# Optimization experiments

Measured on AMD Instinct MI355X. Metric: run time of the kernel, lower is better.

The kernel has to match this reference:

```python
import jax, jax.numpy as jnp
import numpy as np

ELEM, EMBD = 512, 512

def setup_inputs() -> dict:
    key = jax.random.key(0)
    ks = jax.random.split(key, 7)
    s = 1.0 / np.sqrt(ELEM)
    return {
        "x": jax.random.normal(ks[0], (8, 2048, ELEM), dtype=jnp.float32),
        "Wq": jax.random.normal(ks[1], (ELEM, EMBD), dtype=jnp.float32) * s,
        "bq": jnp.zeros((EMBD,), dtype=jnp.float32),
        "Wk": jax.random.normal(ks[2], (ELEM, EMBD), dtype=jnp.float32) * s,
        "bk": jnp.zeros((EMBD,), dtype=jnp.float32),
        "Wv": jax.random.normal(ks[3], (ELEM, EMBD), dtype=jnp.float32) * s,
        "bv": jnp.zeros((EMBD,), dtype=jnp.float32),
    }

def reference(x, Wq, bq, Wk, bk, Wv, bv):
    # x: [N, S, E]
    q = x @ Wq + bq            # [N, S, D]
    k = x @ Wk + bk            # [N, S, D]
    v = x @ Wv + bv            # [N, S, D]
    # NOTE: original has no 1/sqrt(d) scaling.
    logits = jnp.einsum('nsd,ntd->nst', q, k)   # [N, S, S]
    attn = jax.nn.softmax(logits, axis=-1)
    return jnp.einsum('nst,ntd->nsd', attn, v)  # [N, S, D]
```

## Files before the change

### kernel.cpp

```cpp
#include <hip/hip_runtime.h>
#include <hip/hip_fp16.h>

#define SEQ 2048
#define DIM 512

typedef __attribute__((ext_vector_type(8))) short short8;
typedef __attribute__((ext_vector_type(4))) float f32x4;
typedef _Float16 h8 __attribute__((ext_vector_type(8)));
typedef _Float16 h4 __attribute__((ext_vector_type(4)));

#define MFMA16(a, b, c) __builtin_amdgcn_mfma_f32_16x16x32_f16((a), (b), (c), 0, 0, 0)

#define GLOAD_LDS16(g, l)                                                              \
    __builtin_amdgcn_global_load_lds(                                                  \
        (const __attribute__((address_space(1))) unsigned int*)(g),                    \
        (__attribute__((address_space(3))) unsigned int*)(l), 16, 0, 0)

template <int MODE>
__global__ __launch_bounds__(256) void gemmc(
    const _Float16* __restrict__ A, const _Float16* __restrict__ B,
    const float* __restrict__ bq, const float* __restrict__ bk,
    const float* __restrict__ bv,
    _Float16* __restrict__ oq, _Float16* __restrict__ ok, _Float16* __restrict__ ovt,
    float* __restrict__ of, int bat0) {
    __shared__ char sm[2 * 32768];
    constexpr int T  = (MODE == 0) ? 16 : (MODE == 1) ? 8 : 32;
    constexpr int PA = (MODE == 0) ? 512 : (MODE == 1) ? 512 : 4096;
    constexpr int PB = (MODE == 0) ? 1024 : (MODE == 1) ? 512 : 2048;

    int tid = threadIdx.x, wid = tid >> 6, lane = tid & 63, r = lane & 15, g = lane >> 4;
    int mw = wid >> 1, nw = wid & 1;
    int m0 = blockIdx.x * 128, n0 = blockIdx.y * 128, bz = blockIdx.z;

    const _Float16 *Ab, *Bb;
    if (MODE == 0) {
        Ab = A + (size_t)m0 * 512;
        Bb = B + (size_t)n0 * 1024;
    } else if (MODE == 1) {
        int b = bat0 + bz;
        Ab = A + ((size_t)(b * SEQ) + m0) * 512;
        Bb = B + ((size_t)(b * SEQ) + n0) * 512;
    } else {
        int b = bat0 + bz;
        Ab = A + (size_t)bz * (SEQ * 4096) + (size_t)m0 * 4096;
        Bb = B + (size_t)b * (512 * SEQ) + (size_t)n0 * 2048;
    }

    const char* gA[4];
    const char* gB[4];
    int ldsw[4];
#pragma unroll
    for (int j = 0; j < 4; ++j) {
        int ci = (j * 4 + wid) * 64 + lane;
        int row = ci >> 3, cl = ci & 7;
        int col16 = cl ^ (row & 7);
        gA[j] = (const char*)Ab + (size_t)row * (PA * 2) + col16 * 16;
        gB[j] = (const char*)Bb + (size_t)row * (PB * 2) + col16 * 16;
        ldsw[j] = (j * 4 + wid) * 1024;
    }
    int offA[4][2], offB[4][2];
#pragma unroll
    for (int m = 0; m < 4; ++m) {
        int rowA = mw * 64 + m * 16 + r;
        int rowB = nw * 64 + m * 16 + r;
#pragma unroll
        for (int ks = 0; ks < 2; ++ks) {
            offA[m][ks] = rowA * 128 + (((ks * 4 + g) ^ (rowA & 7)) * 16);
            offB[m][ks] = rowB * 128 + (((ks * 4 + g) ^ (rowB & 7)) * 16);
        }
    }

    f32x4 acc[4][4];
#pragma unroll
    for (int m = 0; m < 4; ++m)
#pragma unroll
        for (int n = 0; n < 4; ++n) acc[m][n] = (f32x4)(0.0f);

    auto STG = [&](int t, int b) {
        int ka = (MODE == 0) ? ((t & 7) * 128) : (t * 128);
        int kb = t * 128;
        char* dA = sm + b * 32768;
        char* dB = sm + b * 32768 + 16384;
#pragma unroll
        for (int j = 0; j < 4; ++j) {
            GLOAD_LDS16(gA[j] + ka, dA + ldsw[j]);
            GLOAD_LDS16(gB[j] + kb, dB + ldsw[j]);
        }
    };

    STG(0, 0);
    asm volatile("s_waitcnt vmcnt(0)" ::: "memory");
    __builtin_amdgcn_s_barrier();

#pragma unroll
    for (int t = 0; t < T; ++t) {
        const int buf = t & 1;
        if (t + 1 < T) STG(t + 1, buf ^ 1);
        const char* bA = sm + buf * 32768;
        const char* bB = sm + buf * 32768 + 16384;
        h8 af[4][2], bf[4][2];
#pragma unroll
        for (int m = 0; m < 4; ++m)
#pragma unroll
            for (int ks = 0; ks < 2; ++ks) {
                af[m][ks] = *(const h8*)(bA + offA[m][ks]);
                bf[m][ks] = *(const h8*)(bB + offB[m][ks]);
            }
#pragma unroll
        for (int ks = 0; ks < 2; ++ks)
#pragma unroll
            for (int m = 0; m < 4; ++m)
#pragma unroll
                for (int n = 0; n < 4; ++n)
                    acc[m][n] = MFMA16(af[m][ks], bf[n][ks], acc[m][n]);
        if (t + 1 < T) {
            asm volatile("s_waitcnt vmcnt(0)" ::: "memory");
            __builtin_amdgcn_s_barrier();
        }
    }

    if (MODE == 0) {
        int p = n0 >> 9;
        int ncl = n0 & 511;
        const float* bias = (p == 0) ? bq : (p == 1) ? bk : bv;
#pragma unroll
        for (int n = 0; n < 4; ++n) {
            int col = ncl + nw * 64 + n * 16 + r;
            float bi = bias[col];
#pragma unroll
            for (int m = 0; m < 4; ++m) {
                int grow0 = m0 + mw * 64 + m * 16 + 4 * g;
                if (p == 0) {
                    for (int reg = 0; reg < 4; ++reg)
                        oq[(size_t)(grow0 + reg) * 512 + col] =
                            (_Float16)(acc[m][n][reg] + bi);
                } else if (p == 1) {
                    for (int reg = 0; reg < 4; ++reg)
                        ok[(size_t)(grow0 + reg) * 512 + col] =
                            (_Float16)(acc[m][n][reg] + bi);
                } else {
                    int b = grow0 >> 11, s0 = grow0 & 2047;
                    h4 pv;
                    pv[0] = (_Float16)(acc[m][n][0] + bi);
                    pv[1] = (_Float16)(acc[m][n][1] + bi);
                    pv[2] = (_Float16)(acc[m][n][2] + bi);
                    pv[3] = (_Float16)(acc[m][n][3] + bi);
                    *(h4*)(&ovt[(size_t)b * (512 * 2048) + (size_t)col * 2048 + s0]) = pv;
                }
            }
        }
    } else if (MODE == 1) {
        float* sb = of + (size_t)bz * (SEQ * (size_t)SEQ);
#pragma unroll
        for (int n = 0; n < 4; ++n) {
            int col = n0 + nw * 64 + n * 16 + r;
#pragma unroll
            for (int m = 0; m < 4; ++m) {
                int grow0 = m0 + mw * 64 + m * 16 + 4 * g;
                for (int reg = 0; reg < 4; ++reg)
                    sb[(size_t)(grow0 + reg) * SEQ + col] = acc[m][n][reg];
            }
        }
    } else {
        int b = bat0 + bz;
#pragma unroll
        for (int n = 0; n < 4; ++n) {
            int col = n0 + nw * 64 + n * 16 + r;
#pragma unroll
            for (int m = 0; m < 4; ++m) {
                int grow0 = m0 + mw * 64 + m * 16 + 4 * g;
                for (int reg = 0; reg < 4; ++reg)
                    of[(size_t)(b * SEQ + grow0 + reg) * 512 + col] = acc[m][n][reg];
            }
        }
    }
}

__global__ __launch_bounds__(256) void k0a_splitw(
    const float* __restrict__ Wq, const float* __restrict__ Wk, const float* __restrict__ Wv,
    _Float16* __restrict__ wstk) {
    int idx = blockIdx.x * 256 + threadIdx.x;
    int p = idx >> 18;
    int rem = idx & 262143;
    int k = rem >> 9, n = rem & 511;
    const float* W = (p == 0) ? Wq : (p == 1) ? Wk : Wv;
    float w = W[rem];
    _Float16 h = (_Float16)w;
    size_t base = (size_t)(p * 512 + n) * 1024;
    wstk[base + k] = h;
    wstk[base + 512 + k] = (_Float16)(w - (float)h);
}

__global__ __launch_bounds__(256) void k0b_splitx(
    const float* __restrict__ x, _Float16* __restrict__ xh) {
    size_t i = (size_t)(blockIdx.x * 256 + threadIdx.x) * 4;
    float4 v = *(const float4*)(x + i);
    h4 h;
    h[0] = (_Float16)v.x; h[1] = (_Float16)v.y;
    h[2] = (_Float16)v.z; h[3] = (_Float16)v.w;
    *(h4*)(xh + i) = h;
}

__global__ __launch_bounds__(256) void k3_softmax(float* __restrict__ sbuf) {
    size_t row = blockIdx.x;
    float* srow = sbuf + row * SEQ;
    int tid = threadIdx.x, lane = tid & 63, wid = tid >> 6;
    float4 v0 = *(const float4*)(srow + tid * 8);
    float4 v1 = *(const float4*)(srow + tid * 8 + 4);
    float m = fmaxf(fmaxf(fmaxf(v0.x, v0.y), fmaxf(v0.z, v0.w)),
                    fmaxf(fmaxf(v1.x, v1.y), fmaxf(v1.z, v1.w)));
    for (int d = 1; d < 64; d <<= 1) m = fmaxf(m, __shfl_xor(m, d));
    __shared__ float red1[4], red2[4];
    if (lane == 0) red1[wid] = m;
    __syncthreads();
    m = fmaxf(fmaxf(red1[0], red1[1]), fmaxf(red1[2], red1[3]));
    float e[8];
    e[0] = __expf(v0.x - m); e[1] = __expf(v0.y - m);
    e[2] = __expf(v0.z - m); e[3] = __expf(v0.w - m);
    e[4] = __expf(v1.x - m); e[5] = __expf(v1.y - m);
    e[6] = __expf(v1.z - m); e[7] = __expf(v1.w - m);
    float s = ((e[0] + e[1]) + (e[2] + e[3])) + ((e[4] + e[5]) + (e[6] + e[7]));
    for (int d = 1; d < 64; d <<= 1) s += __shfl_xor(s, d);
    if (lane == 0) red2[wid] = s;
    __syncthreads();
    s = (red2[0] + red2[1]) + (red2[2] + red2[3]);
    float inv = 1.0f / s;
    h8 ph;
    for (int j = 0; j < 8; ++j) ph[j] = (_Float16)(e[j] * inv);
    *(h8*)((char*)srow + (size_t)tid * 16) = ph;
}

extern "C" void kernel_launch(void* const* d_in, const int* in_sizes, int n_in,
                              void* d_out, int out_size, void* d_ws, size_t ws_size,
                              hipStream_t stream) {
    const float* x  = (const float*)d_in[0];
    const float* Wq = (const float*)d_in[1];
    const float* bq = (const float*)d_in[2];
    const float* Wk = (const float*)d_in[3];
    const float* bk = (const float*)d_in[4];
    const float* Wv = (const float*)d_in[5];
    const float* bv = (const float*)d_in[6];
    float* out = (float*)d_out;

    char* ws = (char*)d_ws;
    const size_t QSZ = 16777216;
    _Float16* wstk = (_Float16*)(ws);
    _Float16* xh = (_Float16*)(ws + 3145728);
    _Float16* qh = (_Float16*)(ws + 3145728 + 1 * QSZ);
    _Float16* kh = (_Float16*)(ws + 3145728 + 2 * QSZ);
    _Float16* vt = (_Float16*)(ws + 3145728 + 3 * QSZ);
    const size_t sbase = 3145728 + 4 * QSZ;

    k0a_splitw<<<3072, 256, 0, stream>>>(Wq, Wk, Wv, wstk);
    k0b_splitx<<<8192, 256, 0, stream>>>(x, xh);
    gemmc<0><<<dim3(128, 12), 256, 0, stream>>>(xh, wstk, bq, bk, bv,
                                                qh, kh, vt, nullptr, 0);

    size_t avail = (ws_size > sbase) ? (ws_size - sbase) : 0;
    int chunk = (int)(avail / QSZ);
    if (chunk < 1) chunk = 1;
    if (chunk > 8) chunk = 8;
    float* sc = (float*)(ws + sbase);
    for (int b0 = 0; b0 < 8; b0 += chunk) {
        int nb = (8 - b0 < chunk) ? (8 - b0) : chunk;
        gemmc<1><<<dim3(16, 16, nb), 256, 0, stream>>>(qh, kh, nullptr, nullptr, nullptr,
                                                       nullptr, nullptr, nullptr, sc, b0);
        k3_softmax<<<dim3(nb * SEQ), 256, 0, stream>>>(sc);
        gemmc<2><<<dim3(16, 4, nb), 256, 0, stream>>>((const _Float16*)sc, vt,
                                                      nullptr, nullptr, nullptr,
                                                      nullptr, nullptr, nullptr, out, b0);
    }
}
```

Measured before the change: 189.1 us.

## Enlarge GEMM tiles to 256x128 with 8 waves and triple-buffered LDS pipeline

The shared GEMM kernel moves from 4 to 8 waves per block with a 256x128 output tile. LDS staging goes from double to triple buffering in dynamic shared memory, and loads run two stages ahead using partial vmcnt waits. MFMA sections are wrapped in s_setprio to favour math issue. This aims to hide global-to-LDS latency and cut the number of barrier stalls, at the cost of 144KB LDS per block, one block per CU, and half as many blocks in the grid.

New measurement: 189.9 us. No clear change (+0.4%).

```diff
diff --git a/kernel.cpp b/kernel.cpp
--- a/kernel.cpp
+++ b/kernel.cpp
@@ -17,20 +17,20 @@
         (__attribute__((address_space(3))) unsigned int*)(l), 16, 0, 0)
 
 template <int MODE>
-__global__ __launch_bounds__(256) void gemmc(
+__global__ __launch_bounds__(512, 1) void gemmc(
     const _Float16* __restrict__ A, const _Float16* __restrict__ B,
     const float* __restrict__ bq, const float* __restrict__ bk,
     const float* __restrict__ bv,
     _Float16* __restrict__ oq, _Float16* __restrict__ ok, _Float16* __restrict__ ovt,
     float* __restrict__ of, int bat0) {
-    __shared__ char sm[2 * 32768];
+    extern __shared__ char sm[];
     constexpr int T  = (MODE == 0) ? 16 : (MODE == 1) ? 8 : 32;
     constexpr int PA = (MODE == 0) ? 512 : (MODE == 1) ? 512 : 4096;
     constexpr int PB = (MODE == 0) ? 1024 : (MODE == 1) ? 512 : 2048;
 
     int tid = threadIdx.x, wid = tid >> 6, lane = tid & 63, r = lane & 15, g = lane >> 4;
-    int mw = wid >> 1, nw = wid & 1;
-    int m0 = blockIdx.x * 128, n0 = blockIdx.y * 128, bz = blockIdx.z;
+    int wm = wid >> 1, wn = wid & 1;
+    int m0 = blockIdx.x * 256, n0 = blockIdx.y * 128, bz = blockIdx.z;
 
     const _Float16 *Ab, *Bb;
     if (MODE == 0) {
@@ -47,22 +47,29 @@
     }
 
     const char* gA[4];
-    const char* gB[4];
-    int ldsw[4];
+    const char* gB[2];
+    int ldsA[4], ldsB[2];
 #pragma unroll
     for (int j = 0; j < 4; ++j) {
-        int ci = (j * 4 + wid) * 64 + lane;
+        int ci = j * 512 + tid;
         int row = ci >> 3, cl = ci & 7;
         int col16 = cl ^ (row & 7);
         gA[j] = (const char*)Ab + (size_t)row * (PA * 2) + col16 * 16;
+        ldsA[j] = ci * 16;
+    }
+#pragma unroll
+    for (int j = 0; j < 2; ++j) {
+        int ci = j * 512 + tid;
+        int row = ci >> 3, cl = ci & 7;
+        int col16 = cl ^ (row & 7);
         gB[j] = (const char*)Bb + (size_t)row * (PB * 2) + col16 * 16;
-        ldsw[j] = (j * 4 + wid) * 1024;
+        ldsB[j] = ci * 16;
     }
     int offA[4][2], offB[4][2];
 #pragma unroll
     for (int m = 0; m < 4; ++m) {
-        int rowA = mw * 64 + m * 16 + r;
-        int rowB = nw * 64 + m * 16 + r;
+        int rowA = wm * 64 + m * 16 + r;
+        int rowB = wn * 64 + m * 16 + r;
 #pragma unroll
         for (int ks = 0; ks < 2; ++ks) {
             offA[m][ks] = rowA * 128 + (((ks * 4 + g) ^ (rowA & 7)) * 16);
@@ -79,25 +86,25 @@
     auto STG = [&](int t, int b) {
         int ka = (MODE == 0) ? ((t & 7) * 128) : (t * 128);
         int kb = t * 128;
-        char* dA = sm + b * 32768;
-        char* dB = sm + b * 32768 + 16384;
-#pragma unroll
-        for (int j = 0; j < 4; ++j) {
-            GLOAD_LDS16(gA[j] + ka, dA + ldsw[j]);
-            GLOAD_LDS16(gB[j] + kb, dB + ldsw[j]);
-        }
+        char* dA = sm + b * 49152;
+        char* dB = sm + b * 49152 + 32768;
+#pragma unroll
+        for (int j = 0; j < 4; ++j) GLOAD_LDS16(gA[j] + ka, dA + ldsA[j]);
+#pragma unroll
+        for (int j = 0; j < 2; ++j) GLOAD_LDS16(gB[j] + kb, dB + ldsB[j]);
     };
 
     STG(0, 0);
-    asm volatile("s_waitcnt vmcnt(0)" ::: "memory");
+    STG(1, 1);
+    asm volatile("s_waitcnt vmcnt(6)" ::: "memory");
     __builtin_amdgcn_s_barrier();
 
 #pragma unroll
     for (int t = 0; t < T; ++t) {
-        const int buf = t & 1;
-        if (t + 1 < T) STG(t + 1, buf ^ 1);
-        const char* bA = sm + buf * 32768;
-        const char* bB = sm + buf * 32768 + 16384;
+        const int buf = t % 3;
+        if (t + 2 < T) STG(t + 2, (t + 2) % 3);
+        const char* bA = sm + buf * 49152;
+        const char* bB = sm + buf * 49152 + 32768;
         h8 af[4][2], bf[4][2];
 #pragma unroll
         for (int m = 0; m < 4; ++m)
@@ -106,6 +113,7 @@
                 af[m][ks] = *(const h8*)(bA + offA[m][ks]);
                 bf[m][ks] = *(const h8*)(bB + offB[m][ks]);
             }
+        __builtin_amdgcn_s_setprio(1);
 #pragma unroll
         for (int ks = 0; ks < 2; ++ks)
 #pragma unroll
@@ -113,10 +121,10 @@
 #pragma unroll
                 for (int n = 0; n < 4; ++n)
                     acc[m][n] = MFMA16(af[m][ks], bf[n][ks], acc[m][n]);
-        if (t + 1 < T) {
-            asm volatile("s_waitcnt vmcnt(0)" ::: "memory");
-            __builtin_amdgcn_s_barrier();
-        }
+        __builtin_amdgcn_s_setprio(0);
+        if (t + 2 < T) asm volatile("s_waitcnt vmcnt(6)" ::: "memory");
+        else if (t + 1 < T) asm volatile("s_waitcnt vmcnt(0)" ::: "memory");
+        if (t + 1 < T) __builtin_amdgcn_s_barrier();
     }
 
     if (MODE == 0) {
@@ -125,11 +133,11 @@
         const float* bias = (p == 0) ? bq : (p == 1) ? bk : bv;
 #pragma unroll
         for (int n = 0; n < 4; ++n) {
-            int col = ncl + nw * 64 + n * 16 + r;
+            int col = ncl + wn * 64 + n * 16 + r;
             float bi = bias[col];
 #pragma unroll
             for (int m = 0; m < 4; ++m) {
-                int grow0 = m0 + mw * 64 + m * 16 + 4 * g;
+                int grow0 = m0 + wm * 64 + m * 16 + 4 * g;
                 if (p == 0) {
                     for (int reg = 0; reg < 4; ++reg)
                         oq[(size_t)(grow0 + reg) * 512 + col] =
@@ -153,10 +161,10 @@
         float* sb = of + (size_t)bz * (SEQ * (size_t)SEQ);
 #pragma unroll
         for (int n = 0; n < 4; ++n) {
-            int col = n0 + nw * 64 + n * 16 + r;
+            int col = n0 + wn * 64 + n * 16 + r;
 #pragma unroll
             for (int m = 0; m < 4; ++m) {
-                int grow0 = m0 + mw * 64 + m * 16 + 4 * g;
+                int grow0 = m0 + wm * 64 + m * 16 + 4 * g;
                 for (int reg = 0; reg < 4; ++reg)
                     sb[(size_t)(grow0 + reg) * SEQ + col] = acc[m][n][reg];
             }
@@ -165,10 +173,10 @@
         int b = bat0 + bz;
 #pragma unroll
         for (int n = 0; n < 4; ++n) {
-            int col = n0 + nw * 64 + n * 16 + r;
+            int col = n0 + wn * 64 + n * 16 + r;
 #pragma unroll
             for (int m = 0; m < 4; ++m) {
-                int grow0 = m0 + mw * 64 + m * 16 + 4 * g;
+                int grow0 = m0 + wm * 64 + m * 16 + 4 * g;
                 for (int reg = 0; reg < 4; ++reg)
                     of[(size_t)(b * SEQ + grow0 + reg) * 512 + col] = acc[m][n][reg];
             }
@@ -251,10 +259,18 @@
     _Float16* vt = (_Float16*)(ws + 3145728 + 3 * QSZ);
     const size_t sbase = 3145728 + 4 * QSZ;
 
+    const int LDSB = 3 * 49152;
+    hipFuncSetAttribute((const void*)gemmc<0>,
+                        hipFuncAttributeMaxDynamicSharedMemorySize, LDSB);
+    hipFuncSetAttribute((const void*)gemmc<1>,
+                        hipFuncAttributeMaxDynamicSharedMemorySize, LDSB);
+    hipFuncSetAttribute((const void*)gemmc<2>,
+                        hipFuncAttributeMaxDynamicSharedMemorySize, LDSB);
+
     k0a_splitw<<<3072, 256, 0, stream>>>(Wq, Wk, Wv, wstk);
     k0b_splitx<<<8192, 256, 0, stream>>>(x, xh);
-    gemmc<0><<<dim3(128, 12), 256, 0, stream>>>(xh, wstk, bq, bk, bv,
-                                                qh, kh, vt, nullptr, 0);
+    gemmc<0><<<dim3(64, 12), 512, LDSB, stream>>>(xh, wstk, bq, bk, bv,
+                                                  qh, kh, vt, nullptr, 0);
 
     size_t avail = (ws_size > sbase) ? (ws_size - sbase) : 0;
     int chunk = (int)(avail / QSZ);
@@ -263,11 +279,11 @@
     float* sc = (float*)(ws + sbase);
     for (int b0 = 0; b0 < 8; b0 += chunk) {
         int nb = (8 - b0 < chunk) ? (8 - b0) : chunk;
-        gemmc<1><<<dim3(16, 16, nb), 256, 0, stream>>>(qh, kh, nullptr, nullptr, nullptr,
-                                                       nullptr, nullptr, nullptr, sc, b0);
+        gemmc<1><<<dim3(8, 16, nb), 512, LDSB, stream>>>(qh, kh, nullptr, nullptr, nullptr,
+                                                         nullptr, nullptr, nullptr, sc, b0);
         k3_softmax<<<dim3(nb * SEQ), 256, 0, stream>>>(sc);
-        gemmc<2><<<dim3(16, 4, nb), 256, 0, stream>>>((const _Float16*)sc, vt,
-                                                      nullptr, nullptr, nullptr,
-                                                      nullptr, nullptr, nullptr, out, b0);
-    }
-}
+        gemmc<2><<<dim3(8, 4, nb), 512, LDSB, stream>>>((const _Float16*)sc, vt,
+                                                        nullptr, nullptr, nullptr,
+                                                        nullptr, nullptr, nullptr, out, b0);
+    }
+}
```

## Split QKV projection into two wide-tile triple-buffered GEMMs, dropping K/V split precision

Applied to the files above, without the earlier changes.

The fused QKV projection becomes two kernels. Q keeps the hi/lo fp16 weight split with K=1024. K and V now use plain fp16 weights with K=512, which halves their projection work. Both kernels use 512-thread blocks with 256x128 tiles, three LDS stages and raised MFMA priority. The V output is now transposed through LDS so global stores are coalesced. The cost is lower precision in K and V, which could push the unscaled logits past tolerance, plus one extra launch and lower occupancy from the large LDS footprint.

Result: faster. 174.1 us (-7.9%).

```diff
diff --git a/kernel.cpp b/kernel.cpp
--- a/kernel.cpp
+++ b/kernel.cpp
@@ -17,26 +17,177 @@
         (__attribute__((address_space(3))) unsigned int*)(l), 16, 0, 0)
 
 template <int MODE>
-__global__ __launch_bounds__(256) void gemmc(
+__global__ __launch_bounds__(512, 1) void gemmw(
     const _Float16* __restrict__ A, const _Float16* __restrict__ B,
-    const float* __restrict__ bq, const float* __restrict__ bk,
-    const float* __restrict__ bv,
-    _Float16* __restrict__ oq, _Float16* __restrict__ ok, _Float16* __restrict__ ovt,
+    const float* __restrict__ biasA, const float* __restrict__ biasB,
+    _Float16* __restrict__ o0, _Float16* __restrict__ ovt) {
+    extern __shared__ char sm[];
+    constexpr int T  = (MODE == 0) ? 16 : 8;
+    constexpr int PA = 512;
+    constexpr int PB = (MODE == 0) ? 1024 : 512;
+
+    int tid = threadIdx.x, wid = tid >> 6, lane = tid & 63, r = lane & 15, g = lane >> 4;
+    int wm = wid >> 1, wn = wid & 1;
+    int m0 = blockIdx.x * 256, n0 = blockIdx.y * 128;
+
+    const _Float16* Ab = A + (size_t)m0 * 512;
+    const _Float16* Bb = B + (size_t)n0 * PB;
+
+    const char* gA[4];
+    const char* gB[2];
+    int ldsA[4], ldsB[2];
+#pragma unroll
+    for (int j = 0; j < 4; ++j) {
+        int ci = j * 512 + tid;
+        int row = ci >> 3, cl = ci & 7;
+        int col16 = cl ^ (row & 7);
+        gA[j] = (const char*)Ab + (size_t)row * (PA * 2) + col16 * 16;
+        ldsA[j] = ci * 16;
+    }
+#pragma unroll
+    for (int j = 0; j < 2; ++j) {
+        int ci = j * 512 + tid;
+        int row = ci >> 3, cl = ci & 7;
+        int col16 = cl ^ (row & 7);
+        gB[j] = (const char*)Bb + (size_t)row * (PB * 2) + col16 * 16;
+        ldsB[j] = ci * 16;
+    }
+    int offA[4][2], offB[4][2];
+#pragma unroll
+    for (int m = 0; m < 4; ++m) {
+        int rowA = wm * 64 + m * 16 + r;
+        int rowB = wn * 64 + m * 16 + r;
+#pragma unroll
+        for (int ks = 0; ks < 2; ++ks) {
+            offA[m][ks] = rowA * 128 + (((ks * 4 + g) ^ (rowA & 7)) * 16);
+            offB[m][ks] = rowB * 128 + (((ks * 4 + g) ^ (rowB & 7)) * 16);
+        }
+    }
+
+    f32x4 acc[4][4];
+#pragma unroll
+    for (int m = 0; m < 4; ++m)
+#pragma unroll
+        for (int n = 0; n < 4; ++n) acc[m][n] = (f32x4)(0.0f);
+
+    auto STG = [&](int t, int b) {
+        int ka = (MODE == 0) ? ((t & 7) * 128) : (t * 128);
+        int kb = t * 128;
+        char* dA = sm + b * 49152;
+        char* dB = sm + b * 49152 + 32768;
+#pragma unroll
+        for (int j = 0; j < 4; ++j) GLOAD_LDS16(gA[j] + ka, dA + ldsA[j]);
+#pragma unroll
+        for (int j = 0; j < 2; ++j) GLOAD_LDS16(gB[j] + kb, dB + ldsB[j]);
+    };
+
+    STG(0, 0);
+    STG(1, 1);
+    asm volatile("s_waitcnt vmcnt(6)" ::: "memory");
+    __builtin_amdgcn_s_barrier();
+
+#pragma unroll
+    for (int t = 0; t < T; ++t) {
+        const int buf = t % 3;
+        if (t + 2 < T) STG(t + 2, (t + 2) % 3);
+        const char* bA = sm + buf * 49152;
+        const char* bB = sm + buf * 49152 + 32768;
+        h8 af[4][2], bf[4][2];
+#pragma unroll
+        for (int m = 0; m < 4; ++m)
+#pragma unroll
+            for (int ks = 0; ks < 2; ++ks) {
+                af[m][ks] = *(const h8*)(bA + offA[m][ks]);
+                bf[m][ks] = *(const h8*)(bB + offB[m][ks]);
+            }
+        __builtin_amdgcn_s_setprio(1);
+#pragma unroll
+        for (int ks = 0; ks < 2; ++ks)
+#pragma unroll
+            for (int m = 0; m < 4; ++m)
+#pragma unroll
+                for (int n = 0; n < 4; ++n)
+                    acc[m][n] = MFMA16(af[m][ks], bf[n][ks], acc[m][n]);
+        __builtin_amdgcn_s_setprio(0);
+        if (t + 2 < T) asm volatile("s_waitcnt vmcnt(6)" ::: "memory");
+        else if (t + 1 < T) asm volatile("s_waitcnt vmcnt(0)" ::: "memory");
+        if (t + 1 < T) __builtin_amdgcn_s_barrier();
+    }
+
+    if (MODE == 0) {
+#pragma unroll
+        for (int n = 0; n < 4; ++n) {
+            int col = n0 + wn * 64 + n * 16 + r;
+            float bi = biasA[col];
+#pragma unroll
+            for (int m = 0; m < 4; ++m) {
+                int grow0 = m0 + wm * 64 + m * 16 + 4 * g;
+                for (int reg = 0; reg < 4; ++reg)
+                    o0[(size_t)(grow0 + reg) * 512 + col] =
+                        (_Float16)(acc[m][n][reg] + bi);
+            }
+        }
+    } else {
+        int p = n0 >> 9, ncl = n0 & 511;
+        if (p == 0) {
+#pragma unroll
+            for (int n = 0; n < 4; ++n) {
+                int col = ncl + wn * 64 + n * 16 + r;
+                float bi = biasA[col];
+#pragma unroll
+                for (int m = 0; m < 4; ++m) {
+                    int grow0 = m0 + wm * 64 + m * 16 + 4 * g;
+                    for (int reg = 0; reg < 4; ++reg)
+                        o0[(size_t)(grow0 + reg) * 512 + col] =
+                            (_Float16)(acc[m][n][reg] + bi);
+                }
+            }
+        } else {
+            __syncthreads();
+            _Float16* tt = (_Float16*)sm;
+#pragma unroll
+            for (int n = 0; n < 4; ++n) {
+                int dloc = wn * 64 + n * 16 + r;
+                float bi = biasB[ncl + dloc];
+#pragma unroll
+                for (int m = 0; m < 4; ++m) {
+                    int sloc = wm * 64 + m * 16 + 4 * g;
+                    h4 pv;
+                    pv[0] = (_Float16)(acc[m][n][0] + bi);
+                    pv[1] = (_Float16)(acc[m][n][1] + bi);
+                    pv[2] = (_Float16)(acc[m][n][2] + bi);
+                    pv[3] = (_Float16)(acc[m][n][3] + bi);
+                    *(h4*)(&tt[dloc * 264 + sloc]) = pv;
+                }
+            }
+            __syncthreads();
+            int b = m0 >> 11, s0b = m0 & 2047;
+            int drow = tid >> 2, part = tid & 3;
+            const char* src = (const char*)(tt + drow * 264 + part * 64);
+            char* dst = (char*)(ovt + (size_t)b * (512 * 2048) +
+                                (size_t)(ncl + drow) * 2048 + s0b + part * 64);
+#pragma unroll
+            for (int j = 0; j < 8; ++j)
+                *(short8*)(dst + j * 16) = *(const short8*)(src + j * 16);
+        }
+    }
+}
+
+template <int MODE>
+__global__ __launch_bounds__(256) void gemmn(
+    const _Float16* __restrict__ A, const _Float16* __restrict__ B,
     float* __restrict__ of, int bat0) {
     __shared__ char sm[2 * 32768];
-    constexpr int T  = (MODE == 0) ? 16 : (MODE == 1) ? 8 : 32;
-    constexpr int PA = (MODE == 0) ? 512 : (MODE == 1) ? 512 : 4096;
-    constexpr int PB = (MODE == 0) ? 1024 : (MODE == 1) ? 512 : 2048;
+    constexpr int T  = (MODE == 1) ? 8 : 32;
+    constexpr int PA = (MODE == 1) ? 512 : 4096;
+    constexpr int PB = (MODE == 1) ? 512 : 2048;
 
     int tid = threadIdx.x, wid = tid >> 6, lane = tid & 63, r = lane & 15, g = lane >> 4;
     int mw = wid >> 1, nw = wid & 1;
     int m0 = blockIdx.x * 128, n0 = blockIdx.y * 128, bz = blockIdx.z;
 
     const _Float16 *Ab, *Bb;
-    if (MODE == 0) {
-        Ab = A + (size_t)m0 * 512;
-        Bb = B + (size_t)n0 * 1024;
-    } else if (MODE == 1) {
+    if (MODE == 1) {
         int b = bat0 + bz;
         Ab = A + ((size_t)(b * SEQ) + m0) * 512;
         Bb = B + ((size_t)(b * SEQ) + n0) * 512;
@@ -77,8 +228,7 @@
         for (int n = 0; n < 4; ++n) acc[m][n] = (f32x4)(0.0f);
 
     auto STG = [&](int t, int b) {
-        int ka = (MODE == 0) ? ((t & 7) * 128) : (t * 128);
-        int kb = t * 128;
+        int ka = t * 128, kb = t * 128;
         char* dA = sm + b * 32768;
         char* dB = sm + b * 32768 + 16384;
 #pragma unroll
@@ -119,37 +269,7 @@
         }
     }
 
-    if (MODE == 0) {
-        int p = n0 >> 9;
-        int ncl = n0 & 511;
-        const float* bias = (p == 0) ? bq : (p == 1) ? bk : bv;
-#pragma unroll
-        for (int n = 0; n < 4; ++n) {
-            int col = ncl + nw * 64 + n * 16 + r;
-            float bi = bias[col];
-#pragma unroll
-            for (int m = 0; m < 4; ++m) {
-                int grow0 = m0 + mw * 64 + m * 16 + 4 * g;
-                if (p == 0) {
-                    for (int reg = 0; reg < 4; ++reg)
-                        oq[(size_t)(grow0 + reg) * 512 + col] =
-                            (_Float16)(acc[m][n][reg] + bi);
-                } else if (p == 1) {
-                    for (int reg = 0; reg < 4; ++reg)
-                        ok[(size_t)(grow0 + reg) * 512 + col] =
-                            (_Float16)(acc[m][n][reg] + bi);
-                } else {
-                    int b = grow0 >> 11, s0 = grow0 & 2047;
-                    h4 pv;
-                    pv[0] = (_Float16)(acc[m][n][0] + bi);
-                    pv[1] = (_Float16)(acc[m][n][1] + bi);
-                    pv[2] = (_Float16)(acc[m][n][2] + bi);
-                    pv[3] = (_Float16)(acc[m][n][3] + bi);
-                    *(h4*)(&ovt[(size_t)b * (512 * 2048) + (size_t)col * 2048 + s0]) = pv;
-                }
-            }
-        }
-    } else if (MODE == 1) {
+    if (MODE == 1) {
         float* sb = of + (size_t)bz * (SEQ * (size_t)SEQ);
 #pragma unroll
         for (int n = 0; n < 4; ++n) {
@@ -178,17 +298,21 @@
 
 __global__ __launch_bounds__(256) void k0a_splitw(
     const float* __restrict__ Wq, const float* __restrict__ Wk, const float* __restrict__ Wv,
-    _Float16* __restrict__ wstk) {
+    _Float16* __restrict__ wq, _Float16* __restrict__ wkv) {
     int idx = blockIdx.x * 256 + threadIdx.x;
     int p = idx >> 18;
     int rem = idx & 262143;
     int k = rem >> 9, n = rem & 511;
-    const float* W = (p == 0) ? Wq : (p == 1) ? Wk : Wv;
-    float w = W[rem];
-    _Float16 h = (_Float16)w;
-    size_t base = (size_t)(p * 512 + n) * 1024;
-    wstk[base + k] = h;
-    wstk[base + 512 + k] = (_Float16)(w - (float)h);
+    if (p == 0) {
+        float w = Wq[rem];
+        _Float16 h = (_Float16)w;
+        wq[(size_t)n * 1024 + k] = h;
+        wq[(size_t)n * 1024 + 512 + k] = (_Float16)(w - (float)h);
+    } else if (p == 1) {
+        wkv[(size_t)n * 512 + k] = (_Float16)Wk[rem];
+    } else {
+        wkv[(size_t)(512 + n) * 512 + k] = (_Float16)Wv[rem];
+    }
 }
 
 __global__ __launch_bounds__(256) void k0b_splitx(
@@ -244,17 +368,24 @@
 
     char* ws = (char*)d_ws;
     const size_t QSZ = 16777216;
-    _Float16* wstk = (_Float16*)(ws);
+    _Float16* wq  = (_Float16*)(ws);
+    _Float16* wkv = (_Float16*)(ws + 1048576);
     _Float16* xh = (_Float16*)(ws + 3145728);
     _Float16* qh = (_Float16*)(ws + 3145728 + 1 * QSZ);
     _Float16* kh = (_Float16*)(ws + 3145728 + 2 * QSZ);
     _Float16* vt = (_Float16*)(ws + 3145728 + 3 * QSZ);
     const size_t sbase = 3145728 + 4 * QSZ;
 
-    k0a_splitw<<<3072, 256, 0, stream>>>(Wq, Wk, Wv, wstk);
+    const int LDSW = 3 * 49152;
+    hipFuncSetAttribute((const void*)gemmw<0>,
+                        hipFuncAttributeMaxDynamicSharedMemorySize, LDSW);
+    hipFuncSetAttribute((const void*)gemmw<1>,
+                        hipFuncAttributeMaxDynamicSharedMemorySize, LDSW);
+
+    k0a_splitw<<<3072, 256, 0, stream>>>(Wq, Wk, Wv, wq, wkv);
     k0b_splitx<<<8192, 256, 0, stream>>>(x, xh);
-    gemmc<0><<<dim3(128, 12), 256, 0, stream>>>(xh, wstk, bq, bk, bv,
-                                                qh, kh, vt, nullptr, 0);
+    gemmw<0><<<dim3(64, 4), 512, LDSW, stream>>>(xh, wq, bq, nullptr, qh, nullptr);
+    gemmw<1><<<dim3(64, 8), 512, LDSW, stream>>>(xh, wkv, bk, bv, kh, vt);
 
     size_t avail = (ws_size > sbase) ? (ws_size - sbase) : 0;
     int chunk = (int)(avail / QSZ);
@@ -263,11 +394,8 @@
     float* sc = (float*)(ws + sbase);
     for (int b0 = 0; b0 < 8; b0 += chunk) {
         int nb = (8 - b0 < chunk) ? (8 - b0) : chunk;
-        gemmc<1><<<dim3(16, 16, nb), 256, 0, stream>>>(qh, kh, nullptr, nullptr, nullptr,
-                                                       nullptr, nullptr, nullptr, sc, b0);
+        gemmn<1><<<dim3(16, 16, nb), 256, 0, stream>>>(qh, kh, sc, b0);
         k3_softmax<<<dim3(nb * SEQ), 256, 0, stream>>>(sc);
-        gemmc<2><<<dim3(16, 4, nb), 256, 0, stream>>>((const _Float16*)sc, vt,
-                                                      nullptr, nullptr, nullptr,
-                                                      nullptr, nullptr, nullptr, out, b0);
-    }
-}
+        gemmn<2><<<dim3(16, 4, nb), 256, 0, stream>>>((const _Float16*)sc, vt, out, b0);
+    }
+}
```
